# Optimization experiments

Measured on AMD Instinct MI355X. Metric: run time of the kernel, lower is better.

The kernel has to match this reference:

```python
import jax, jax.numpy as jnp
import numpy as np
import math

H = 128      # hidden_channels
R = 32       # num_rbf
N = 4096     # atoms
E = 65536    # edges
CU = 4.5     # cutoff_upper (cutoff_lower = 0)
ALPHA = 5.0 / CU
MEANS = jnp.linspace(math.exp(-CU), 1.0, R, dtype=jnp.float32)
BETA = jnp.float32((2.0 / R * (1.0 - math.exp(-CU))) ** -2)
EPS = 1e-5


def _ln(x, g, b):
    mu = x.mean(-1, keepdims=True)
    var = ((x - mu) ** 2).mean(-1, keepdims=True)
    return (x - mu) * jax.lax.rsqrt(var + EPS) * g + b


def setup_inputs() -> dict:
    key = jax.random.key(0)
    ks = jax.random.split(key, 20)
    f32 = jnp.float32

    def w(i, shape):
        return jax.random.normal(ks[i], shape, f32) / np.float32(np.sqrt(shape[-1]))

    return {
        "edge_vec": jax.random.normal(ks[0], (E, 3), f32) * 1.5,
        "emb_w": w(1, (128, H)),
        "emb2_w": w(2, (H, 2 * H)), "emb2_b": jnp.zeros((H,), f32),
        "dp1_w": w(3, (H, R)), "dp1_b": jnp.zeros((H,), f32),
        "dp2_w": w(4, (H, R)), "dp2_b": jnp.zeros((H,), f32),
        "dp3_w": w(5, (H, R)), "dp3_b": jnp.zeros((H,), f32),
        "lt0_w": w(6, (H, H)), "lt1_w": w(7, (H, H)), "lt2_w": w(8, (H, H)),
        "ls0_w": w(9, (2 * H, H)), "ls0_b": jnp.zeros((2 * H,), f32),
        "ls1_w": w(10, (3 * H, 2 * H)), "ls1_b": jnp.zeros((3 * H,), f32),
        "init_g": jnp.ones((H,), f32), "init_b": jnp.zeros((H,), f32),
        "lin_w": w(11, (H, 3 * H)), "lin_b": jnp.zeros((H,), f32),
        "outn_g": jnp.ones((3 * H,), f32), "outn_b": jnp.zeros((3 * H,), f32),
        "ol1_w": w(12, (H // 2, H)), "ol1_b": jnp.zeros((H // 2,), f32),
        "ol2_w": w(13, (1, H // 2)), "ol2_b": jnp.zeros((1,), f32),
        "z": jax.random.randint(ks[14], (N,), 0, 128, dtype=jnp.int32),
        "edge_index": jax.random.randint(ks[15], (2, E), 0, N, dtype=jnp.int32),
    }


def reference(edge_vec, emb_w, emb2_w, emb2_b, dp1_w, dp1_b, dp2_w, dp2_b,
              dp3_w, dp3_b, lt0_w, lt1_w, lt2_w, ls0_w, ls0_b, ls1_w, ls1_b,
              init_g, init_b, lin_w, lin_b, outn_g, outn_b, ol1_w, ol1_b,
              ol2_w, ol2_b, z, edge_index):
    n = z.shape[0]
    src, dst = edge_index[0], edge_index[1]

    d = jnp.sqrt((edge_vec ** 2).sum(-1))                 # (E,)
    vn = edge_vec / d[:, None]                             # unit edge vectors
    cut = jnp.where(d < CU, 0.5 * (jnp.cos(jnp.pi * d / CU) + 1.0), 0.0)
    # expnorm RBF
    rbf = cut[:, None] * jnp.exp(-BETA * (jnp.exp(-ALPHA * d)[:, None] - MEANS) ** 2)  # (E,R)

    # atomic-number message Zij = emb2(cat(emb(z_i), emb(z_j)))
    zpair = jnp.concatenate([emb_w[z[src]], emb_w[z[dst]]], -1)  # (E,2H)
    zij = zpair @ emb2_w.T + emb2_b                              # (E,H)
    c = cut[:, None] * zij                                       # cutoff * Zij, (E,H)

    w1 = (rbf @ dp1_w.T + dp1_b) * c    # scalar channel weights (E,H)
    w2 = (rbf @ dp2_w.T + dp2_b) * c
    w3 = (rbf @ dp3_w.T + dp3_b) * c

    eye = jnp.eye(3, dtype=edge_vec.dtype)
    zero = jnp.zeros_like(vn[:, 0])
    skew = jnp.stack([zero, -vn[:, 2], vn[:, 1],
                      vn[:, 2], zero, -vn[:, 0],
                      -vn[:, 1], vn[:, 0], zero], 1).reshape(-1, 3, 3)  # (E,3,3)
    outer = vn[:, :, None] * vn[:, None, :]
    sym = outer - ((vn ** 2).sum(-1) / 3.0)[:, None, None] * eye        # traceless sym (E,3,3)

    seg = lambda a: jax.ops.segment_sum(a, src, num_segments=n)
    I0 = seg(w1)[:, :, None, None] * eye                                # (N,H,3,3)
    A0 = seg(w2[:, :, None, None] * skew[:, None, :, :])                # (N,H,3,3)
    S0 = seg(w3[:, :, None, None] * sym[:, None, :, :])                 # (N,H,3,3)

    tn = ((I0 + A0 + S0) ** 2).sum((-2, -1))                            # tensor_norm, (N,H)
    nrm = _ln(tn, init_g, init_b)
    h = jax.nn.silu(nrm @ ls0_w.T + ls0_b)
    scal = jax.nn.silu(h @ ls1_w.T + ls1_b).reshape(n, H, 3)            # per-channel gates

    I1 = jnp.einsum('nhxy,gh->ngxy', I0, lt0_w) * scal[..., 0][..., None, None]
    A1 = jnp.einsum('nhxy,gh->ngxy', A0, lt1_w) * scal[..., 1][..., None, None]
    S1 = jnp.einsum('nhxy,gh->ngxy', S0, lt2_w) * scal[..., 2][..., None, None]

    x = jnp.concatenate([(I1 ** 2).sum((-2, -1)),
                         (A1 ** 2).sum((-2, -1)),
                         (S1 ** 2).sum((-2, -1))], -1)                  # (N,3H)
    x = _ln(x, outn_g, outn_b)
    s1 = x @ lin_w.T + lin_b
    s2 = jax.nn.silu(s1) @ ol1_w.T + ol1_b
    s3 = jax.nn.silu(s2) @ ol2_w.T + ol2_b                              # per-atom energy (N,1)
    return s3
```

## Files before the change

kernel.cpp:

```cpp
#include <hip/hip_runtime.h>
#include <math.h>

#define NH_TOT 524288
#define N_ATOM 4096
#define N_EDGE 65536

typedef __attribute__((ext_vector_type(8))) short bf16x8;
typedef __attribute__((ext_vector_type(4))) float f32x4;

__device__ __forceinline__ unsigned short f2bf(float f) {
    unsigned u = __builtin_bit_cast(unsigned, f);
    unsigned r = (u + 0x7fffu + ((u >> 16) & 1u)) >> 16;
    return (unsigned short)r;
}
__device__ __forceinline__ float silu(float v) { return v / (1.0f + __expf(-v)); }

#define WB_LS1 32768
#define WB_LT0 131072
#define WB_LT1 147456
#define WB_LT2 163840
#define WB_DP  180224

__global__ __launch_bounds__(256) void k_setup(
    const float* __restrict__ emb_w, const float* __restrict__ emb2_w,
    const int* __restrict__ ei,
    const float* __restrict__ ls0_w, const float* __restrict__ ls1_w,
    const float* __restrict__ lt0_w, const float* __restrict__ lt1_w,
    const float* __restrict__ lt2_w,
    const float* __restrict__ dp1_w, const float* __restrict__ dp2_w,
    const float* __restrict__ dp3_w,
    float* __restrict__ U1, float* __restrict__ U2,
    int* __restrict__ cnt, unsigned short* __restrict__ wb) {
    const int bx = blockIdx.x, tid = threadIdx.x;
    if (bx < 64) {
        __shared__ float se[2][128];
        const int t = bx * 2 + (tid >> 7), h = tid & 127, half = tid >> 7;
        se[half][h] = emb_w[t * 128 + h];
        __syncthreads();
        float u1 = 0.f, u2 = 0.f;
        const float* row = emb2_w + h * 256;
#pragma unroll 8
        for (int k = 0; k < 128; k++) {
            u1 += se[half][k] * row[k];
            u2 += se[half][k] * row[128 + k];
        }
        U1[t * 128 + h] = u1;
        U2[t * 128 + h] = u2;
    } else if (bx < 320) {
        const int e = (bx - 64) * 256 + tid;
        atomicAdd(&cnt[ei[e]], 1);
    } else {
        const int base = (bx - 320) * 1024 + tid * 4;
        const float* src;
        int off;
        if (base < 32768)       { src = ls0_w; off = 0; }
        else if (base < 131072) { src = ls1_w; off = 32768; }
        else if (base < 147456) { src = lt0_w; off = 131072; }
        else if (base < 163840) { src = lt1_w; off = 147456; }
        else if (base < 180224) { src = lt2_w; off = 163840; }
        else if (base < 184320) { src = dp1_w; off = 180224; }
        else if (base < 188416) { src = dp2_w; off = 184320; }
        else                    { src = dp3_w; off = 188416; }
        const float4 v = *(const float4*)(src + (base - off));
        unsigned short* o = wb + base;
        o[0] = f2bf(v.x); o[1] = f2bf(v.y); o[2] = f2bf(v.z); o[3] = f2bf(v.w);
    }
}

__global__ __launch_bounds__(256) void k_scan(const int* __restrict__ cnt, int* __restrict__ off) {
    __shared__ int s[256];
    const int t = threadIdx.x;
    int loc[16];
    int run = 0;
#pragma unroll
    for (int i = 0; i < 16; i++) { run += cnt[t * 16 + i]; loc[i] = run; }
    s[t] = run;
    __syncthreads();
    for (int d = 1; d < 256; d <<= 1) {
        const int add = (t >= d) ? s[t - d] : 0;
        __syncthreads();
        s[t] += add;
        __syncthreads();
    }
    const int base = s[t] - run;
    if (t == 0) off[0] = 0;
#pragma unroll
    for (int i = 0; i < 16; i++) off[t * 16 + i + 1] = base + loc[i];
}

__global__ __launch_bounds__(256) void k_edge(
    const float* __restrict__ edge_vec, const int* __restrict__ ei,
    const int* __restrict__ z, const int* __restrict__ off,
    int* __restrict__ cursor,
    unsigned short* __restrict__ rbf_bf, float4* __restrict__ geom,
    int* __restrict__ u2off) {
    const int e = blockIdx.x * 256 + threadIdx.x;
    const int src = ei[e];
    const int pos = off[src] + atomicAdd(&cursor[src], 1);

    const float evx = edge_vec[3 * e + 0];
    const float evy = edge_vec[3 * e + 1];
    const float evz = edge_vec[3 * e + 2];
    const float d = sqrtf(evx * evx + evy * evy + evz * evz);
    const float inv = 1.0f / d;
    const float cut = (d < 4.5f) ? 0.5f * (__cosf(0.6981317007977318f * d) + 1.0f) : 0.0f;
    geom[pos] = make_float4(evx * inv, evy * inv, evz * inv, cut);
    u2off[pos] = z[ei[N_EDGE + e]] << 7;

    const float expd = __expf(-1.1111111111111112f * d);
    const float m0 = 0.011108996538242306f;
    const float dm = (1.0f - m0) * (1.0f / 31.0f);
    const float tb = 0.0625f * (1.0f - m0);
    const float beta = 1.0f / (tb * tb);
    unsigned int rb[16];
#pragma unroll
    for (int r = 0; r < 16; r++) {
        const float df0 = expd - (m0 + (float)(2 * r) * dm);
        const float df1 = expd - (m0 + (float)(2 * r + 1) * dm);
        const unsigned lo = f2bf(cut * __expf(-beta * df0 * df0));
        const unsigned hi = f2bf(cut * __expf(-beta * df1 * df1));
        rb[r] = lo | (hi << 16);
    }
    uint4* dst = (uint4*)(rbf_bf + (size_t)pos * 32);
#pragma unroll
    for (int j = 0; j < 4; j++)
        dst[j] = make_uint4(rb[4 * j], rb[4 * j + 1], rb[4 * j + 2], rb[4 * j + 3]);
}

__global__ __launch_bounds__(256) void k_node(
    const int* __restrict__ z, const int* __restrict__ off,
    const unsigned short* __restrict__ rbf_bf, const float4* __restrict__ geom,
    const int* __restrict__ u2off,
    const float* __restrict__ U1, const float* __restrict__ U2,
    const float* __restrict__ emb2_b,
    const float* __restrict__ dp1_b, const float* __restrict__ dp2_b,
    const float* __restrict__ dp3_b,
    const unsigned short* __restrict__ wb,
    const float* __restrict__ init_g, const float* __restrict__ init_b,
    unsigned short* __restrict__ acc_bf, unsigned short* __restrict__ nrm_bf) {
    const int tid = threadIdx.x;
    const int wave = tid >> 6, lane = tid & 63, lm = lane & 15, lq = lane >> 4;
    const int nb = blockIdx.x * 8;

    const unsigned short* dpw = wb + WB_DP;
    bf16x8 bfr[3][2];
    float bhc[2], bk1[2], bk2[2], bk3[2];
    int cols[2];
#pragma unroll
    for (int t = 0; t < 2; t++) {
        const int col = wave * 32 + t * 16 + lm;
        cols[t] = col;
        bhc[t] = emb2_b[col];
        bk1[t] = dp1_b[col]; bk2[t] = dp2_b[col]; bk3[t] = dp3_b[col];
#pragma unroll
        for (int k = 0; k < 3; k++)
            bfr[k][t] = *(const bf16x8*)(dpw + k * 4096 + col * 32 + lq * 8);
    }

    __shared__ float redS[8][4];
    __shared__ float redQ[8][4];

    float tnA[8], tnB[8];

    for (int nn = 0; nn < 8; nn++) {
        const int n = nb + nn;
        const int beg = off[n];
        const int En = off[n + 1] - beg;
        const int zoff = z[n] << 7;
        const float u1c0 = U1[zoff + cols[0]];
        const float u1c1 = U1[zoff + cols[1]];

        float part[10][2];
#pragma unroll
        for (int p = 0; p < 10; p++) { part[p][0] = 0.f; part[p][1] = 0.f; }

        for (int mi = 0; mi < En; mi += 16) {
            const int arow = beg + min(mi + lm, En - 1);
            const bf16x8 af = *(const bf16x8*)(rbf_bf + (size_t)arow * 32 + lq * 8);
            f32x4 c[3][2];
#pragma unroll
            for (int k = 0; k < 3; k++)
#pragma unroll
                for (int t = 0; t < 2; t++)
                    c[k][t] = __builtin_amdgcn_mfma_f32_16x16x32_bf16(
                        af, bfr[k][t], (f32x4){0.f, 0.f, 0.f, 0.f}, 0, 0, 0);
#pragma unroll
            for (int r = 0; r < 4; r++) {
                const int er = mi + lq * 4 + r;
                const bool valid = er < En;
                const int p = beg + (valid ? er : 0);
                const float4 g = geom[p];
                const int u2o = u2off[p];
#pragma unroll
                for (int t = 0; t < 2; t++) {
                    const float u2v = U2[u2o + cols[t]];
                    const float u1h = (t == 0) ? u1c0 : u1c1;
                    const float cc = valid ? g.w * (u1h + u2v + bhc[t]) : 0.f;
                    const float w1 = (c[0][t][r] + bk1[t]) * cc;
                    const float w2 = (c[1][t][r] + bk2[t]) * cc;
                    const float w3 = (c[2][t][r] + bk3[t]) * cc;
                    part[0][t] += w1;
                    part[1][t] += w2 * g.x; part[2][t] += w2 * g.y; part[3][t] += w2 * g.z;
                    const float tx = w3 * g.x, ty = w3 * g.y;
                    part[4][t] += tx * g.x; part[5][t] += tx * g.y; part[6][t] += tx * g.z;
                    part[7][t] += ty * g.y; part[8][t] += ty * g.z; part[9][t] += w3 * g.z * g.z;
                }
            }
        }

#pragma unroll
        for (int p = 0; p < 10; p++)
#pragma unroll
            for (int t = 0; t < 2; t++) {
                float v = part[p][t];
                v += __shfl_xor(v, 16, 64);
                v += __shfl_xor(v, 32, 64);
                part[p][t] = v;
            }
        if (lq == 0) {
#pragma unroll
            for (int p = 0; p < 10; p++)
#pragma unroll
                for (int t = 0; t < 2; t++)
                    acc_bf[(size_t)p * NH_TOT + n * 128 + cols[t]] = f2bf(part[p][t]);
        }

        float tn[2];
#pragma unroll
        for (int t = 0; t < 2; t++) {
            const float aI = part[0][t];
            const float axv = part[1][t], ayv = part[2][t], azv = part[3][t];
            const float mxx = part[4][t], mxy = part[5][t], mxz = part[6][t];
            const float myy = part[7][t], myz = part[8][t], mzz = part[9][t];
            const float tr3 = (mxx + myy + mzz) * (1.0f / 3.0f);
            const float t00 = aI + mxx - tr3;
            const float t11 = aI + myy - tr3;
            const float t22 = aI + mzz - tr3;
            tn[t] = t00 * t00 + t11 * t11 + t22 * t22 +
                    2.0f * (mxy * mxy + azv * azv + mxz * mxz + ayv * ayv + myz * myz + axv * axv);
        }
        tnA[nn] = tn[0];
        tnB[nn] = tn[1];

        float s = (lq == 0) ? (tn[0] + tn[1]) : 0.f;
        s += __shfl_xor(s, 1, 64);
        s += __shfl_xor(s, 2, 64);
        s += __shfl_xor(s, 4, 64);
        s += __shfl_xor(s, 8, 64);
        if (lane == 0) redS[nn][wave] = s;
    }
    __syncthreads();

    float dvA[8], dvB[8];
#pragma unroll
    for (int nn = 0; nn < 8; nn++) {
        const float mu = (redS[nn][0] + redS[nn][1] + redS[nn][2] + redS[nn][3]) * (1.0f / 128.0f);
        dvA[nn] = tnA[nn] - mu;
        dvB[nn] = tnB[nn] - mu;
        float q = (lq == 0) ? (dvA[nn] * dvA[nn] + dvB[nn] * dvB[nn]) : 0.f;
        q += __shfl_xor(q, 1, 64);
        q += __shfl_xor(q, 2, 64);
        q += __shfl_xor(q, 4, 64);
        q += __shfl_xor(q, 8, 64);
        if (lane == 0) redQ[nn][wave] = q;
    }
    __syncthreads();

    if (lq == 0) {
        const float g0 = init_g[cols[0]], g1 = init_g[cols[1]];
        const float b0 = init_b[cols[0]], b1 = init_b[cols[1]];
#pragma unroll
        for (int nn = 0; nn < 8; nn++) {
            const float var = (redQ[nn][0] + redQ[nn][1] + redQ[nn][2] + redQ[nn][3]) * (1.0f / 128.0f);
            const float rs = rsqrtf(var + 1e-5f);
            const int n = nb + nn;
            nrm_bf[n * 128 + cols[0]] = f2bf(dvA[nn] * rs * g0 + b0);
            nrm_bf[n * 128 + cols[1]] = f2bf(dvB[nn] * rs * g1 + b1);
        }
    }
}

__global__ __launch_bounds__(256) void k_megatail(
    const unsigned short* __restrict__ nrm_bf, const unsigned short* __restrict__ acc_bf,
    const unsigned short* __restrict__ wb,
    const float* __restrict__ ls0_b, const float* __restrict__ ls1_b,
    const float* __restrict__ outn_g, const float* __restrict__ outn_b,
    const float* __restrict__ lin_w, const float* __restrict__ lin_b,
    const float* __restrict__ ol1_w, const float* __restrict__ ol1_b,
    const float* __restrict__ ol2_w, const float* __restrict__ ol2_b,
    float* __restrict__ out) {
    const int tid = threadIdx.x, wave = tid >> 6, lane = tid & 63;
    const int lm = lane & 15, lq = lane >> 4;
    const int n0 = blockIdx.x * 8;

    __shared__ unsigned short h1[16][280];
    __shared__ float scal_s[8][388];
    __shared__ float xs[8][392];
    __shared__ float ss[8][132];

    {
        f32x4 acc[4];
#pragma unroll
        for (int j = 0; j < 4; j++) acc[j] = (f32x4){0.f, 0.f, 0.f, 0.f};
        const int cbase = wave * 64;
#pragma unroll
        for (int kc = 0; kc < 128; kc += 32) {
            const int arow = n0 + min(lm, 7);
            const bf16x8 af = *(const bf16x8*)(nrm_bf + (size_t)arow * 128 + kc + lq * 8);
#pragma unroll
            for (int sn = 0; sn < 4; sn++) {
                const bf16x8 b = *(const bf16x8*)(wb + (size_t)(cbase + sn * 16 + lm) * 128 + kc + lq * 8);
                acc[sn] = __builtin_amdgcn_mfma_f32_16x16x32_bf16(af, b, acc[sn], 0, 0, 0);
            }
        }
#pragma unroll
        for (int sn = 0; sn < 4; sn++) {
            const int col = cbase + sn * 16 + lm;
            const float bv = ls0_b[col];
#pragma unroll
            for (int r = 0; r < 4; r++)
                h1[lq * 4 + r][col] = f2bf(silu(acc[sn][r] + bv));
        }
    }
    __syncthreads();
    {
        f32x4 acc[6];
#pragma unroll
        for (int j = 0; j < 6; j++) acc[j] = (f32x4){0.f, 0.f, 0.f, 0.f};
        const int cbase = wave * 96;
        const unsigned short* ls1p = wb + WB_LS1;
#pragma unroll 2
        for (int kc = 0; kc < 256; kc += 32) {
            const bf16x8 af = *(const bf16x8*)(&h1[lm][kc + lq * 8]);
#pragma unroll
            for (int sn = 0; sn < 6; sn++) {
                const bf16x8 b = *(const bf16x8*)(ls1p + (size_t)(cbase + sn * 16 + lm) * 256 + kc + lq * 8);
                acc[sn] = __builtin_amdgcn_mfma_f32_16x16x32_bf16(af, b, acc[sn], 0, 0, 0);
            }
        }
#pragma unroll
        for (int sn = 0; sn < 6; sn++) {
            const int col = cbase + sn * 16 + lm;
            const float bv = ls1_b[col];
#pragma unroll
            for (int r = 0; r < 4; r++) {
                const int node = lq * 4 + r;
                if (node < 8) scal_s[node][col] = silu(acc[sn][r] + bv);
            }
        }
    }
    __syncthreads();

    f32x4 e0[2], e1[2], e2[2], trv[2];
#pragma unroll
    for (int sn = 0; sn < 2; sn++) {
        e0[sn] = (f32x4){0.f, 0.f, 0.f, 0.f};
        e1[sn] = (f32x4){0.f, 0.f, 0.f, 0.f};
        e2[sn] = (f32x4){0.f, 0.f, 0.f, 0.f};
        trv[sn] = (f32x4){0.f, 0.f, 0.f, 0.f};
    }
#pragma unroll
    for (int p = 0; p < 10; p++) {
        const unsigned short* A = acc_bf + (size_t)p * NH_TOT;
        const unsigned short* B = wb + (p == 0 ? WB_LT0 : (p < 4 ? WB_LT1 : WB_LT2));
        f32x4 c[2];
        c[0] = (f32x4){0.f, 0.f, 0.f, 0.f};
        c[1] = (f32x4){0.f, 0.f, 0.f, 0.f};
#pragma unroll
        for (int kc = 0; kc < 128; kc += 32) {
            const int arow = n0 + min(lm, 7);
            const bf16x8 af = *(const bf16x8*)(A + (size_t)arow * 128 + kc + lq * 8);
#pragma unroll
            for (int sn = 0; sn < 2; sn++) {
                const bf16x8 b = *(const bf16x8*)(B + (size_t)(wave * 32 + sn * 16 + lm) * 128 + kc + lq * 8);
                c[sn] = __builtin_amdgcn_mfma_f32_16x16x32_bf16(af, b, c[sn], 0, 0, 0);
            }
        }
#pragma unroll
        for (int sn = 0; sn < 2; sn++) {
            if (p == 0)      e0[sn] += c[sn] * c[sn];
            else if (p < 4)  e1[sn] += c[sn] * c[sn];
            else if (p == 4 || p == 7 || p == 9) { e2[sn] += c[sn] * c[sn]; trv[sn] += c[sn]; }
            else             e2[sn] += 2.0f * c[sn] * c[sn];
        }
    }

    if (lq < 2) {
#pragma unroll
        for (int sn = 0; sn < 2; sn++) {
            const int g = wave * 32 + sn * 16 + lm;
#pragma unroll
            for (int r = 0; r < 4; r++) {
                const int node = lq * 4 + r;
                const float s0 = scal_s[node][3 * g + 0];
                const float s1 = scal_s[node][3 * g + 1];
                const float s2 = scal_s[node][3 * g + 2];
                xs[node][g]       = 3.0f * e0[sn][r] * s0 * s0;
                xs[node][128 + g] = 2.0f * e1[sn][r] * s1 * s1;
                const float tr = trv[sn][r];
                xs[node][256 + g] = (e2[sn][r] - tr * tr * (1.0f / 3.0f)) * s2 * s2;
            }
        }
    }
    __syncthreads();

#pragma unroll
    for (int i = 0; i < 2; i++) {
        const int node = wave * 2 + i;
        float v[6];
        float s = 0.f;
#pragma unroll
        for (int j = 0; j < 6; j++) { v[j] = xs[node][lane + 64 * j]; s += v[j]; }
#pragma unroll
        for (int o = 1; o < 64; o <<= 1) s += __shfl_xor(s, o, 64);
        const float mu = s * (1.0f / 384.0f);
        float q = 0.f;
#pragma unroll
        for (int j = 0; j < 6; j++) { v[j] -= mu; q += v[j] * v[j]; }
#pragma unroll
        for (int o = 1; o < 64; o <<= 1) q += __shfl_xor(q, o, 64);
        const float rs = rsqrtf(q * (1.0f / 384.0f) + 1e-5f);
#pragma unroll
        for (int j = 0; j < 6; j++) {
            const int col = lane + 64 * j;
            xs[node][col] = v[j] * rs * outn_g[col] + outn_b[col];
        }
    }
    __syncthreads();

    {
        const int j = tid & 127, half = tid >> 7;
        float a4[4];
        const float lb = lin_b[j];
#pragma unroll
        for (int i = 0; i < 4; i++) a4[i] = lb;
        const float4* wr = (const float4*)(lin_w + j * 384);
#pragma unroll 2
        for (int k4 = 0; k4 < 96; k4++) {
            const float4 w4 = wr[k4];
#pragma unroll
            for (int i = 0; i < 4; i++) {
                const float4 xv = *(const float4*)&xs[half * 4 + i][k4 * 4];
                a4[i] += w4.x * xv.x + w4.y * xv.y + w4.z * xv.z + w4.w * xv.w;
            }
        }
#pragma unroll
        for (int i = 0; i < 4; i++) ss[half * 4 + i][j] = silu(a4[i]);
    }
    __syncthreads();

    {
        const int o = tid & 63, q = tid >> 6;
        float a2v[2];
        const float ob = ol1_b[o];
        a2v[0] = ob; a2v[1] = ob;
        const float4* o4 = (const float4*)(ol1_w + o * 128);
#pragma unroll 4
        for (int k4 = 0; k4 < 32; k4++) {
            const float4 w4 = o4[k4];
#pragma unroll
            for (int i = 0; i < 2; i++) {
                const float4 sv = *(const float4*)&ss[q * 2 + i][k4 * 4];
                a2v[i] += w4.x * sv.x + w4.y * sv.y + w4.z * sv.z + w4.w * sv.w;
            }
        }
        const float w2 = ol2_w[o];
#pragma unroll
        for (int i = 0; i < 2; i++) {
            float v = silu(a2v[i]) * w2;
            for (int s = 32; s > 0; s >>= 1) v += __shfl_down(v, s, 64);
            if (o == 0) out[n0 + q * 2 + i] = v + ol2_b[0];
        }
    }
}

extern "C" void kernel_launch(void* const* d_in, const int* in_sizes, int n_in,
                              void* d_out, int out_size, void* d_ws, size_t ws_size,
                              hipStream_t stream) {
    (void)in_sizes; (void)n_in; (void)out_size; (void)ws_size;
    const float* edge_vec = (const float*)d_in[0];
    const float* emb_w   = (const float*)d_in[1];
    const float* emb2_w  = (const float*)d_in[2];
    const float* emb2_b  = (const float*)d_in[3];
    const float* dp1_w   = (const float*)d_in[4];
    const float* dp1_b   = (const float*)d_in[5];
    const float* dp2_w   = (const float*)d_in[6];
    const float* dp2_b   = (const float*)d_in[7];
    const float* dp3_w   = (const float*)d_in[8];
    const float* dp3_b   = (const float*)d_in[9];
    const float* lt0_w   = (const float*)d_in[10];
    const float* lt1_w   = (const float*)d_in[11];
    const float* lt2_w   = (const float*)d_in[12];
    const float* ls0_w   = (const float*)d_in[13];
    const float* ls0_b   = (const float*)d_in[14];
    const float* ls1_w   = (const float*)d_in[15];
    const float* ls1_b   = (const float*)d_in[16];
    const float* init_g  = (const float*)d_in[17];
    const float* init_b  = (const float*)d_in[18];
    const float* lin_w   = (const float*)d_in[19];
    const float* lin_b   = (const float*)d_in[20];
    const float* outn_g  = (const float*)d_in[21];
    const float* outn_b  = (const float*)d_in[22];
    const float* ol1_w   = (const float*)d_in[23];
    const float* ol1_b   = (const float*)d_in[24];
    const float* ol2_w   = (const float*)d_in[25];
    const float* ol2_b   = (const float*)d_in[26];
    const int* z  = (const int*)d_in[27];
    const int* ei = (const int*)d_in[28];
    float* out = (float*)d_out;

    char* w = (char*)d_ws;
    int*            cnt    = (int*)(w);
    int*            cursor = (int*)(w + 16384);
    int*            off    = (int*)(w + 32768);
    unsigned short* wb     = (unsigned short*)(w + 49408);
    float*          U1     = (float*)(w + 434432);
    float*          U2     = (float*)(w + 499968);
    int*            u2off  = (int*)(w + 565504);
    float4*         geom   = (float4*)(w + 827648);
    unsigned short* rbf_bf = (unsigned short*)(w + 1876224);
    unsigned short* nrm_bf = (unsigned short*)(w + 6070528);
    unsigned short* acc_bf = (unsigned short*)(w + 7119104);

    hipMemsetAsync(w, 0, 32768, stream);
    k_setup<<<dim3(508), dim3(256), 0, stream>>>(emb_w, emb2_w, ei,
                                                 ls0_w, ls1_w, lt0_w, lt1_w, lt2_w,
                                                 dp1_w, dp2_w, dp3_w,
                                                 U1, U2, cnt, wb);
    k_scan<<<dim3(1), dim3(256), 0, stream>>>(cnt, off);
    k_edge<<<dim3(256), dim3(256), 0, stream>>>(edge_vec, ei, z, off, cursor,
                                                rbf_bf, geom, u2off);
    k_node<<<dim3(512), dim3(256), 0, stream>>>(z, off, rbf_bf, geom, u2off, U1, U2,
                                                emb2_b, dp1_b, dp2_b, dp3_b, wb,
                                                init_g, init_b, acc_bf, nrm_bf);
    k_megatail<<<dim3(512), dim3(256), 0, stream>>>(nrm_bf, acc_bf, wb, ls0_b, ls1_b,
                                                    outn_g, outn_b, lin_w, lin_b,
                                                    ol1_w, ol1_b, ol2_w, ol2_b, out);
}
```

Baseline: 246.5 us.

## Split edge RBF work across 8 threads and prefetch weights in megatail

k_edge now uses 8 threads per edge. One thread takes the atomic slot and the others get it by shuffle, and each thread computes and stores 4 RBF values, so 8x as many blocks are launched. k_megatail stages all ten acc_bf slices and nrm_bf rows into LDS up front, and double-buffers the MFMA B-operand loads from global across the k-chunks of the ls0, ls1 and lt GEMMs. The scalar tail loops get larger unroll factors. This adds parallelism and hides load latency in exchange for more registers and LDS (about 24KB more per block), which may reduce occupancy.

Measured after the change: 249.3 us. About the same (+1.1%).

```diff
diff --git a/kernel.cpp b/kernel.cpp
--- a/kernel.cpp
+++ b/kernel.cpp
@@ -94,37 +94,43 @@
     int* __restrict__ cursor,
     unsigned short* __restrict__ rbf_bf, float4* __restrict__ geom,
     int* __restrict__ u2off) {
-    const int e = blockIdx.x * 256 + threadIdx.x;
-    const int src = ei[e];
-    const int pos = off[src] + atomicAdd(&cursor[src], 1);
+    const int idx = blockIdx.x * 256 + threadIdx.x;
+    const int e = idx >> 3, s = idx & 7;
+    const int lane = threadIdx.x & 63;
 
     const float evx = edge_vec[3 * e + 0];
     const float evy = edge_vec[3 * e + 1];
     const float evz = edge_vec[3 * e + 2];
     const float d = sqrtf(evx * evx + evy * evy + evz * evz);
-    const float inv = 1.0f / d;
     const float cut = (d < 4.5f) ? 0.5f * (__cosf(0.6981317007977318f * d) + 1.0f) : 0.0f;
-    geom[pos] = make_float4(evx * inv, evy * inv, evz * inv, cut);
-    u2off[pos] = z[ei[N_EDGE + e]] << 7;
+
+    int pos = 0;
+    if (s == 0) {
+        const int src = ei[e];
+        pos = off[src] + atomicAdd(&cursor[src], 1);
+    }
+    pos = __shfl(pos, lane & 56, 64);
+    if (s == 0) {
+        const float inv = 1.0f / d;
+        geom[pos] = make_float4(evx * inv, evy * inv, evz * inv, cut);
+        u2off[pos] = z[ei[N_EDGE + e]] << 7;
+    }
 
     const float expd = __expf(-1.1111111111111112f * d);
     const float m0 = 0.011108996538242306f;
     const float dm = (1.0f - m0) * (1.0f / 31.0f);
     const float tb = 0.0625f * (1.0f - m0);
     const float beta = 1.0f / (tb * tb);
-    unsigned int rb[16];
-#pragma unroll
-    for (int r = 0; r < 16; r++) {
-        const float df0 = expd - (m0 + (float)(2 * r) * dm);
-        const float df1 = expd - (m0 + (float)(2 * r + 1) * dm);
-        const unsigned lo = f2bf(cut * __expf(-beta * df0 * df0));
-        const unsigned hi = f2bf(cut * __expf(-beta * df1 * df1));
-        rb[r] = lo | (hi << 16);
-    }
-    uint4* dst = (uint4*)(rbf_bf + (size_t)pos * 32);
-#pragma unroll
-    for (int j = 0; j < 4; j++)
-        dst[j] = make_uint4(rb[4 * j], rb[4 * j + 1], rb[4 * j + 2], rb[4 * j + 3]);
+    unsigned rb[2];
+#pragma unroll
+    for (int j = 0; j < 2; j++) {
+        const int r = s * 4 + 2 * j;
+        const float df0 = expd - (m0 + (float)r * dm);
+        const float df1 = expd - (m0 + (float)(r + 1) * dm);
+        rb[j] = (unsigned)f2bf(cut * __expf(-beta * df0 * df0)) |
+                ((unsigned)f2bf(cut * __expf(-beta * df1 * df1)) << 16);
+    }
+    *(uint2*)(rbf_bf + (size_t)pos * 32 + s * 4) = make_uint2(rb[0], rb[1]);
 }
 
 __global__ __launch_bounds__(256) void k_node(
@@ -292,26 +298,51 @@
     const int tid = threadIdx.x, wave = tid >> 6, lane = tid & 63;
     const int lm = lane & 15, lq = lane >> 4;
     const int n0 = blockIdx.x * 8;
-
+    const int ar = (lm < 8) ? lm : 7;
+
+    __shared__ unsigned short accs[10][8][136];
+    __shared__ unsigned short nrms[8][136];
     __shared__ unsigned short h1[16][280];
     __shared__ float scal_s[8][388];
     __shared__ float xs[8][392];
     __shared__ float ss[8][132];
 
+#pragma unroll
+    for (int j = 0; j < 5; j++) {
+        const int i = tid + j * 256;
+        const int row_id = i >> 4, q = i & 15;
+        const int p = row_id >> 3, r = row_id & 7;
+        const uint4 v = *(const uint4*)(acc_bf + (size_t)p * NH_TOT + (size_t)(n0 + r) * 128 + q * 8);
+        *(uint4*)(&accs[p][r][q * 8]) = v;
+    }
+    if (tid < 128) {
+        const int r = tid >> 4, q = tid & 15;
+        *(uint4*)(&nrms[r][q * 8]) = *(const uint4*)(nrm_bf + (size_t)(n0 + r) * 128 + q * 8);
+    }
+    __syncthreads();
+
     {
         f32x4 acc[4];
 #pragma unroll
         for (int j = 0; j < 4; j++) acc[j] = (f32x4){0.f, 0.f, 0.f, 0.f};
         const int cbase = wave * 64;
+        bf16x8 bcur[4], bnxt[4];
+#pragma unroll
+        for (int sn = 0; sn < 4; sn++)
+            bcur[sn] = *(const bf16x8*)(wb + (size_t)(cbase + sn * 16 + lm) * 128 + lq * 8);
 #pragma unroll
         for (int kc = 0; kc < 128; kc += 32) {
-            const int arow = n0 + min(lm, 7);
-            const bf16x8 af = *(const bf16x8*)(nrm_bf + (size_t)arow * 128 + kc + lq * 8);
-#pragma unroll
-            for (int sn = 0; sn < 4; sn++) {
-                const bf16x8 b = *(const bf16x8*)(wb + (size_t)(cbase + sn * 16 + lm) * 128 + kc + lq * 8);
-                acc[sn] = __builtin_amdgcn_mfma_f32_16x16x32_bf16(af, b, acc[sn], 0, 0, 0);
-            }
+            if (kc < 96) {
+#pragma unroll
+                for (int sn = 0; sn < 4; sn++)
+                    bnxt[sn] = *(const bf16x8*)(wb + (size_t)(cbase + sn * 16 + lm) * 128 + kc + 32 + lq * 8);
+            }
+            const bf16x8 af = *(const bf16x8*)(&nrms[ar][kc + lq * 8]);
+#pragma unroll
+            for (int sn = 0; sn < 4; sn++)
+                acc[sn] = __builtin_amdgcn_mfma_f32_16x16x32_bf16(af, bcur[sn], acc[sn], 0, 0, 0);
+#pragma unroll
+            for (int sn = 0; sn < 4; sn++) bcur[sn] = bnxt[sn];
         }
 #pragma unroll
         for (int sn = 0; sn < 4; sn++) {
@@ -323,20 +354,30 @@
         }
     }
     __syncthreads();
+
     {
         f32x4 acc[6];
 #pragma unroll
         for (int j = 0; j < 6; j++) acc[j] = (f32x4){0.f, 0.f, 0.f, 0.f};
         const int cbase = wave * 96;
         const unsigned short* ls1p = wb + WB_LS1;
-#pragma unroll 2
+        bf16x8 bcur[6], bnxt[6];
+#pragma unroll
+        for (int sn = 0; sn < 6; sn++)
+            bcur[sn] = *(const bf16x8*)(ls1p + (size_t)(cbase + sn * 16 + lm) * 256 + lq * 8);
+#pragma unroll
         for (int kc = 0; kc < 256; kc += 32) {
+            if (kc < 224) {
+#pragma unroll
+                for (int sn = 0; sn < 6; sn++)
+                    bnxt[sn] = *(const bf16x8*)(ls1p + (size_t)(cbase + sn * 16 + lm) * 256 + kc + 32 + lq * 8);
+            }
             const bf16x8 af = *(const bf16x8*)(&h1[lm][kc + lq * 8]);
 #pragma unroll
-            for (int sn = 0; sn < 6; sn++) {
-                const bf16x8 b = *(const bf16x8*)(ls1p + (size_t)(cbase + sn * 16 + lm) * 256 + kc + lq * 8);
-                acc[sn] = __builtin_amdgcn_mfma_f32_16x16x32_bf16(af, b, acc[sn], 0, 0, 0);
-            }
+            for (int sn = 0; sn < 6; sn++)
+                acc[sn] = __builtin_amdgcn_mfma_f32_16x16x32_bf16(af, bcur[sn], acc[sn], 0, 0, 0);
+#pragma unroll
+            for (int sn = 0; sn < 6; sn++) bcur[sn] = bnxt[sn];
         }
 #pragma unroll
         for (int sn = 0; sn < 6; sn++) {
@@ -359,29 +400,39 @@
         e2[sn] = (f32x4){0.f, 0.f, 0.f, 0.f};
         trv[sn] = (f32x4){0.f, 0.f, 0.f, 0.f};
     }
-#pragma unroll
-    for (int p = 0; p < 10; p++) {
-        const unsigned short* A = acc_bf + (size_t)p * NH_TOT;
-        const unsigned short* B = wb + (p == 0 ? WB_LT0 : (p < 4 ? WB_LT1 : WB_LT2));
-        f32x4 c[2];
-        c[0] = (f32x4){0.f, 0.f, 0.f, 0.f};
-        c[1] = (f32x4){0.f, 0.f, 0.f, 0.f};
-#pragma unroll
-        for (int kc = 0; kc < 128; kc += 32) {
-            const int arow = n0 + min(lm, 7);
-            const bf16x8 af = *(const bf16x8*)(A + (size_t)arow * 128 + kc + lq * 8);
-#pragma unroll
-            for (int sn = 0; sn < 2; sn++) {
-                const bf16x8 b = *(const bf16x8*)(B + (size_t)(wave * 32 + sn * 16 + lm) * 128 + kc + lq * 8);
-                c[sn] = __builtin_amdgcn_mfma_f32_16x16x32_bf16(af, b, c[sn], 0, 0, 0);
-            }
-        }
-#pragma unroll
-        for (int sn = 0; sn < 2; sn++) {
-            if (p == 0)      e0[sn] += c[sn] * c[sn];
-            else if (p < 4)  e1[sn] += c[sn] * c[sn];
-            else if (p == 4 || p == 7 || p == 9) { e2[sn] += c[sn] * c[sn]; trv[sn] += c[sn]; }
-            else             e2[sn] += 2.0f * c[sn] * c[sn];
+    {
+        const int coff = wave * 32;
+        f32x4 c0, c1;
+        bf16x8 bcur0, bcur1, bnxt0, bnxt1;
+        {
+            const unsigned short* B = wb + WB_LT0;
+            bcur0 = *(const bf16x8*)(B + (size_t)(coff + lm) * 128 + lq * 8);
+            bcur1 = *(const bf16x8*)(B + (size_t)(coff + 16 + lm) * 128 + lq * 8);
+        }
+#pragma unroll
+        for (int it = 0; it < 40; it++) {
+            const int p = it >> 2, k = it & 3;
+            if (it < 39) {
+                const int pn = (it + 1) >> 2, kn = (it + 1) & 3;
+                const unsigned short* B = wb + (pn == 0 ? WB_LT0 : (pn < 4 ? WB_LT1 : WB_LT2));
+                bnxt0 = *(const bf16x8*)(B + (size_t)(coff + lm) * 128 + kn * 32 + lq * 8);
+                bnxt1 = *(const bf16x8*)(B + (size_t)(coff + 16 + lm) * 128 + kn * 32 + lq * 8);
+            }
+            if (k == 0) { c0 = (f32x4){0.f, 0.f, 0.f, 0.f}; c1 = (f32x4){0.f, 0.f, 0.f, 0.f}; }
+            const bf16x8 af = *(const bf16x8*)(&accs[p][ar][k * 32 + lq * 8]);
+            c0 = __builtin_amdgcn_mfma_f32_16x16x32_bf16(af, bcur0, c0, 0, 0, 0);
+            c1 = __builtin_amdgcn_mfma_f32_16x16x32_bf16(af, bcur1, c1, 0, 0, 0);
+            bcur0 = bnxt0; bcur1 = bnxt1;
+            if (k == 3) {
+                if (p == 0)      { e0[0] += c0 * c0; e0[1] += c1 * c1; }
+                else if (p < 4)  { e1[0] += c0 * c0; e1[1] += c1 * c1; }
+                else if (p == 4 || p == 7 || p == 9) {
+                    e2[0] += c0 * c0; e2[1] += c1 * c1;
+                    trv[0] += c0;     trv[1] += c1;
+                } else {
+                    e2[0] += 2.0f * c0 * c0; e2[1] += 2.0f * c1 * c1;
+                }
+            }
         }
     }
 
@@ -435,7 +486,7 @@
 #pragma unroll
         for (int i = 0; i < 4; i++) a4[i] = lb;
         const float4* wr = (const float4*)(lin_w + j * 384);
-#pragma unroll 2
+#pragma unroll 8
         for (int k4 = 0; k4 < 96; k4++) {
             const float4 w4 = wr[k4];
 #pragma unroll
@@ -455,7 +506,7 @@
         const float ob = ol1_b[o];
         a2v[0] = ob; a2v[1] = ob;
         const float4* o4 = (const float4*)(ol1_w + o * 128);
-#pragma unroll 4
+#pragma unroll 8
         for (int k4 = 0; k4 < 32; k4++) {
             const float4 w4 = o4[k4];
 #pragma unroll
@@ -528,8 +579,8 @@
                                                  dp1_w, dp2_w, dp3_w,
                                                  U1, U2, cnt, wb);
     k_scan<<<dim3(1), dim3(256), 0, stream>>>(cnt, off);
-    k_edge<<<dim3(256), dim3(256), 0, stream>>>(edge_vec, ei, z, off, cursor,
-                                                rbf_bf, geom, u2off);
+    k_edge<<<dim3(2048), dim3(256), 0, stream>>>(edge_vec, ei, z, off, cursor,
+                                                 rbf_bf, geom, u2off);
     k_node<<<dim3(512), dim3(256), 0, stream>>>(z, off, rbf_bf, geom, u2off, U1, U2,
                                                 emb2_b, dp1_b, dp2_b, dp3_b, wb,
                                                 init_g, init_b, acc_bf, nrm_bf);
```
